# Optimization experiments

Measured on AMD Instinct MI355X. Metric: run time of the kernel, lower is better.

The kernel has to match this reference:

```python
import jax, jax.numpy as jnp
import numpy as np

N_QUBITS = 8    # out_channels = number of wires
KERNEL = 4      # kernel_size
N_LAYERS = 3
PAD = 1
STRIDE = 1


def _gate_rx(t):
    c = jnp.cos(t / 2).astype(jnp.complex64)
    s = (-1j) * jnp.sin(t / 2).astype(jnp.complex64)
    return jnp.stack([jnp.stack([c, s]), jnp.stack([s, c])])


def _gate_ry(t):
    c = jnp.cos(t / 2).astype(jnp.complex64)
    s = jnp.sin(t / 2).astype(jnp.complex64)
    return jnp.stack([jnp.stack([c, -s]), jnp.stack([s, c])])


def _gate_rz(t):
    tc = t.astype(jnp.complex64)
    e0 = jnp.exp(-0.5j * tc)
    e1 = jnp.exp(0.5j * tc)
    z = jnp.zeros_like(e0)
    return jnp.stack([jnp.stack([e0, z]), jnp.stack([z, e1])])


def _apply1(state, gate, q):
    # state: (W, 2, ..., 2); shared 2x2 gate on qubit axis 1+q
    s = jnp.moveaxis(state, 1 + q, -1)
    s = jnp.einsum('...a,ba->...b', s, gate)
    return jnp.moveaxis(s, -1, 1 + q)


def _apply_ry_batched(state, theta, q):
    # per-window RY angles theta: (W,)
    c = jnp.cos(theta / 2)
    s = jnp.sin(theta / 2)
    g = jnp.stack([jnp.stack([c, -s], -1), jnp.stack([s, c], -1)], -2).astype(jnp.complex64)  # (W,2,2)
    st = jnp.moveaxis(state, 1 + q, -1)
    st = jnp.einsum('w...a,wba->w...b', st, g)
    return jnp.moveaxis(st, -1, 1 + q)


def _apply_cnot(state, c, t):
    # control qubit c, target qubit t (axes 1+c, 1+t)
    s = jnp.moveaxis(state, 1 + c, 1)
    ta = 2 + t if t < c else 1 + t
    s = jnp.moveaxis(s, ta, 2)
    s = jnp.stack([s[:, 0], jnp.flip(s[:, 1], axis=1)], axis=1)
    s = jnp.moveaxis(s, 2, ta)
    return jnp.moveaxis(s, 1, 1 + c)


def _ansatz(state, w):
    # custom_ansatz: per wire j: RX(w[j]); CNOT; RY(w[j]); CNOT; RZ(w[j]) with ring entanglement
    for j in range(N_QUBITS):
        cw, tw = (j, j + 1) if j < N_QUBITS - 1 else (0, N_QUBITS - 1)
        state = _apply1(state, _gate_rx(w[j]), j)
        state = _apply_cnot(state, cw, tw)
        state = _apply1(state, _gate_ry(w[j]), j)
        state = _apply_cnot(state, cw, tw)
        state = _apply1(state, _gate_rz(w[j]), j)
    return state

_ansatz_ckpt = jax.checkpoint(_ansatz)


@jax.jit
def _circuit(windows, weights):
    # windows: (W, KERNEL); weights: (N_LAYERS+1, N_QUBITS)
    W = windows.shape[0]
    state = jnp.zeros((W,) + (2,) * N_QUBITS, jnp.complex64)
    state = state.at[(slice(None),) + (0,) * N_QUBITS].set(1.0)
    state = _ansatz_ckpt(state, weights[0])
    for k in range(KERNEL):  # 'no_reupload' data encoding, once
        state = _apply_ry_batched(state, windows[:, k], k)
    for i in range(1, N_LAYERS + 1):
        state = _ansatz_ckpt(state, weights[i])
    probs = state.real ** 2 + state.imag ** 2
    evs = []
    for j in range(N_QUBITS):
        axes = tuple(a for a in range(1, N_QUBITS + 1) if a != 1 + j)
        p = probs.sum(axis=axes)  # (W, 2)
        evs.append(p[:, 0] - p[:, 1])
    return jnp.stack(evs, axis=-1)  # (W, N_QUBITS)


def setup_inputs() -> dict:
    key = jax.random.key(0)
    k1, k2 = jax.random.split(key)
    vector = jax.random.normal(k1, (32, 1, 512), jnp.float32)
    weights = jax.random.uniform(k2, (N_LAYERS + 1, N_QUBITS), jnp.float32, 0.0, 2.0 * np.pi)
    return {"vector": vector, "weights": weights}


def reference(vector, weights):
    bs, ch, l = vector.shape
    if ch > 1:
        vector = vector.mean(axis=1, keepdims=True)
    v = jnp.pad(vector[:, 0], ((0, 0), (PAD, PAD)))
    l_out = (l + 2 * PAD - KERNEL) // STRIDE + 1
    idx = jnp.arange(0, l_out, STRIDE)[:, None] + jnp.arange(KERNEL)[None, :]
    windows = v[:, idx].reshape(-1, KERNEL)  # (bs*l_out, KERNEL)
    out = _circuit(windows, weights)
    return out.reshape(bs, l_out, N_QUBITS).transpose(0, 2, 1).astype(jnp.float32)
```

## Files before the change

kernel.cpp:

```cpp
#include <hip/hip_runtime.h>
#include <math.h>


#define DEV __device__ __forceinline__

#define NQ 8
#define LOUT 511
#define LIN 512
#define BS 32

DEV float sx(float v, int m) { return __shfl_xor(v, m, 64); }

template<int J>
DEV void rot_rx(float (&re)[4], float (&im)[4], float c, float s) {
    if constexpr (J == 0) {
        float r0=re[0], i0=im[0], r2=re[2], i2=im[2];
        re[0]=c*r0+s*i2; im[0]=c*i0-s*r2; re[2]=c*r2+s*i0; im[2]=c*i2-s*r0;
        float r1=re[1], i1=im[1], r3=re[3], i3=im[3];
        re[1]=c*r1+s*i3; im[1]=c*i1-s*r3; re[3]=c*r3+s*i1; im[3]=c*i3-s*r1;
    } else if constexpr (J == 1) {
        float r0=re[0], i0=im[0], r1=re[1], i1=im[1];
        re[0]=c*r0+s*i1; im[0]=c*i0-s*r1; re[1]=c*r1+s*i0; im[1]=c*i1-s*r0;
        float r2=re[2], i2=im[2], r3=re[3], i3=im[3];
        re[2]=c*r2+s*i3; im[2]=c*i2-s*r3; re[3]=c*r3+s*i2; im[3]=c*i3-s*r2;
    } else {
        constexpr int m = 1 << (7 - J);
        #pragma unroll
        for (int r = 0; r < 4; ++r) {
            float pre = sx(re[r], m), pim = sx(im[r], m);
            re[r] = c*re[r] + s*pim;
            im[r] = c*im[r] - s*pre;
        }
    }
}

template<int J>
DEV void rot_ry(float (&re)[4], float (&im)[4], float c, float s, int lane) {
    if constexpr (J == 0) {
        float r0=re[0], i0=im[0], r2=re[2], i2=im[2];
        re[0]=c*r0-s*r2; im[0]=c*i0-s*i2; re[2]=s*r0+c*r2; im[2]=s*i0+c*i2;
        float r1=re[1], i1=im[1], r3=re[3], i3=im[3];
        re[1]=c*r1-s*r3; im[1]=c*i1-s*i3; re[3]=s*r1+c*r3; im[3]=s*i1+c*i3;
    } else if constexpr (J == 1) {
        float r0=re[0], i0=im[0], r1=re[1], i1=im[1];
        re[0]=c*r0-s*r1; im[0]=c*i0-s*i1; re[1]=s*r0+c*r1; im[1]=s*i0+c*i1;
        float r2=re[2], i2=im[2], r3=re[3], i3=im[3];
        re[2]=c*r2-s*r3; im[2]=c*i2-s*i3; re[3]=s*r2+c*r3; im[3]=s*i2+c*i3;
    } else {
        constexpr int m = 1 << (7 - J);
        float sg = (lane & m) ? s : -s;
        #pragma unroll
        for (int r = 0; r < 4; ++r) {
            float pre = sx(re[r], m), pim = sx(im[r], m);
            re[r] = c*re[r] + sg*pre;
            im[r] = c*im[r] + sg*pim;
        }
    }
}

template<int J>
DEV void rot_rz(float (&re)[4], float (&im)[4], float c, float s, int lane) {
    if constexpr (J == 0) {
        float t;
        t=re[0]; re[0]=c*t+s*im[0]; im[0]=c*im[0]-s*t;
        t=re[1]; re[1]=c*t+s*im[1]; im[1]=c*im[1]-s*t;
        t=re[2]; re[2]=c*t-s*im[2]; im[2]=c*im[2]+s*t;
        t=re[3]; re[3]=c*t-s*im[3]; im[3]=c*im[3]+s*t;
    } else if constexpr (J == 1) {
        float t;
        t=re[0]; re[0]=c*t+s*im[0]; im[0]=c*im[0]-s*t;
        t=re[2]; re[2]=c*t+s*im[2]; im[2]=c*im[2]-s*t;
        t=re[1]; re[1]=c*t-s*im[1]; im[1]=c*im[1]+s*t;
        t=re[3]; re[3]=c*t-s*im[3]; im[3]=c*im[3]+s*t;
    } else {
        constexpr int m = 1 << (7 - J);
        float sg = (lane & m) ? -s : s;
        #pragma unroll
        for (int r = 0; r < 4; ++r) {
            float t = re[r];
            re[r] = c*t + sg*im[r];
            im[r] = c*im[r] - sg*t;
        }
    }
}

template<int J>
DEV void cnot_w(float (&re)[4], float (&im)[4], int lane) {
    if constexpr (J == 0) {
        float t;
        t=re[2]; re[2]=re[3]; re[3]=t;
        t=im[2]; im[2]=im[3]; im[3]=t;
    } else if constexpr (J == 1) {
        re[1]=sx(re[1],32); im[1]=sx(im[1],32);
        re[3]=sx(re[3],32); im[3]=sx(im[3],32);
    } else if constexpr (J == 7) {
        re[2]=sx(re[2],1); im[2]=sx(im[2],1);
        re[3]=sx(re[3],1); im[3]=sx(im[3],1);
    } else {
        constexpr int mc = 1 << (7 - J);
        constexpr int mt = 1 << (6 - J);
        bool ctrl = (lane & mc) != 0;
        #pragma unroll
        for (int r = 0; r < 4; ++r) {
            float pre = sx(re[r], mt), pim = sx(im[r], mt);
            re[r] = ctrl ? pre : re[r];
            im[r] = ctrl ? pim : im[r];
        }
    }
}

template<int J>
DEV void wire(float (&re)[4], float (&im)[4], float ang, int lane) {
    float s, c;
    sincosf(0.5f*ang, &s, &c);
    rot_rx<J>(re, im, c, s);
    cnot_w<J>(re, im, lane);
    rot_ry<J>(re, im, c, s, lane);
    cnot_w<J>(re, im, lane);
    rot_rz<J>(re, im, c, s, lane);
}

DEV void ansatz(float (&re)[4], float (&im)[4], const float* w, int lane) {
    wire<0>(re, im, w[0], lane);
    wire<1>(re, im, w[1], lane);
    wire<2>(re, im, w[2], lane);
    wire<3>(re, im, w[3], lane);
    wire<4>(re, im, w[4], lane);
    wire<5>(re, im, w[5], lane);
    wire<6>(re, im, w[6], lane);
    wire<7>(re, im, w[7], lane);
}

__global__ __launch_bounds__(64) void kA1(const float* __restrict__ wts,
                                          float2* __restrict__ q) {
    int lane = threadIdx.x;
    int b = blockIdx.x;
    float re[4] = {0.f,0.f,0.f,0.f}, im[4] = {0.f,0.f,0.f,0.f};
    if (lane == 0) re[0] = 1.0f;
    ansatz(re, im, wts, lane);
    if (b & 1) {
        float t;
        t=re[0]; re[0]=-re[2]; re[2]=t;  t=im[0]; im[0]=-im[2]; im[2]=t;
        t=re[1]; re[1]=-re[3]; re[3]=t;  t=im[1]; im[1]=-im[3]; im[3]=t;
    }
    if (b & 2) {
        float t;
        t=re[0]; re[0]=-re[1]; re[1]=t;  t=im[0]; im[0]=-im[1]; im[1]=t;
        t=re[2]; re[2]=-re[3]; re[3]=t;  t=im[2]; im[2]=-im[3]; im[3]=t;
    }
    if (b & 4) {
        bool hi = (lane & 32) != 0;
        #pragma unroll
        for (int r = 0; r < 4; ++r) {
            float pre = sx(re[r],32), pim = sx(im[r],32);
            re[r] = hi ? pre : -pre;
            im[r] = hi ? pim : -pim;
        }
    }
    if (b & 8) {
        bool hi = (lane & 16) != 0;
        #pragma unroll
        for (int r = 0; r < 4; ++r) {
            float pre = sx(re[r],16), pim = sx(im[r],16);
            re[r] = hi ? pre : -pre;
            im[r] = hi ? pim : -pim;
        }
    }
    ansatz(re, im, wts + 8,  lane);
    ansatz(re, im, wts + 16, lane);
    ansatz(re, im, wts + 24, lane);
    #pragma unroll
    for (int r = 0; r < 4; ++r)
        q[b*256 + r*64 + lane] = make_float2(re[r], im[r]);
}

__global__ __launch_bounds__(64) void kA2(const float2* __restrict__ q,
                                          float* __restrict__ S) {
    int lane = threadIdx.x;
    int b  = blockIdx.x >> 4;
    int bp = blockIdx.x & 15;
    float pp[4];
    #pragma unroll
    for (int rr = 0; rr < 4; ++rr) {
        float2 x = q[b*256  + rr*64 + lane];
        float2 y = q[bp*256 + rr*64 + lane];
        pp[rr] = x.x*y.x + x.y*y.y;
    }
    float acc[8];
    acc[0] = (pp[0]+pp[1]) - (pp[2]+pp[3]);
    acc[1] = (pp[0]+pp[2]) - (pp[1]+pp[3]);
    float tot = pp[0]+pp[1]+pp[2]+pp[3];
    acc[2] = (lane & 32) ? -tot : tot;
    acc[3] = (lane & 16) ? -tot : tot;
    acc[4] = (lane &  8) ? -tot : tot;
    acc[5] = (lane &  4) ? -tot : tot;
    acc[6] = (lane &  2) ? -tot : tot;
    acc[7] = (lane &  1) ? -tot : tot;
    #pragma unroll
    for (int j = 0; j < 8; ++j) {
        #pragma unroll
        for (int m = 1; m <= 32; m <<= 1)
            acc[j] += sx(acc[j], m);
    }
    if (lane == 0) {
        #pragma unroll
        for (int j = 0; j < 8; ++j)
            S[j*256 + b*16 + bp] = acc[j];
    }
}

__global__ __launch_bounds__(256) void kB(const float* __restrict__ vec,
                                          const float* __restrict__ S,
                                          float* __restrict__ out) {
    __shared__ float Sl[2048];
    for (int i = threadIdx.x; i < 2048; i += 256) Sl[i] = S[i];
    __syncthreads();
    int o   = blockIdx.x * 256 + threadIdx.x;
    int bat = blockIdx.y;
    if (o >= LOUT) return;
    float cs[4], sn[4];
    #pragma unroll
    for (int k = 0; k < 4; ++k) {
        int p = o + k;
        float x = (p >= 1 && p <= LIN) ? vec[bat*LIN + p - 1] : 0.f;
        sincosf(0.5f*x, &sn[k], &cs[k]);
    }
    float t[16];
    #pragma unroll
    for (int i = 0; i < 16; ++i)
        t[i] = ((i&1)?sn[0]:cs[0]) * ((i&2)?sn[1]:cs[1])
             * ((i&4)?sn[2]:cs[2]) * ((i&8)?sn[3]:cs[3]);
    for (int j = 0; j < 8; ++j) {
        float e = 0.f;
        #pragma unroll
        for (int b = 0; b < 16; ++b) {
            float u = 0.f;
            #pragma unroll
            for (int bp = 0; bp < 16; ++bp)
                u += Sl[j*256 + b*16 + bp] * t[bp];
            e += t[b] * u;
        }
        out[(bat*NQ + j)*LOUT + o] = e;
    }
}

extern "C" void kernel_launch(void* const* d_in, const int* in_sizes, int n_in,
                              void* d_out, int out_size, void* d_ws, size_t ws_size,
                              hipStream_t stream) {
    const float* vec = (const float*)d_in[0];
    const float* wts = (const float*)d_in[1];
    float* out = (float*)d_out;
    float2* q  = (float2*)d_ws;
    float*  S  = (float*)d_ws + 8192;
    kA1<<<16, 64, 0, stream>>>(wts, q);
    kA2<<<256, 64, 0, stream>>>(q, S);
    kB<<<dim3(2, BS), 256, 0, stream>>>(vec, S, out);
}
```

Baseline: 93.96 us.

## Fuse state-prep and overlap kernels, exploit S symmetry, use fast sincos

Merges the two precompute kernels into one 1024-thread block that keeps the 16 basis-state vectors in shared memory and computes only the 136 upper-triangle overlap entries, with off-diagonal terms doubled. The final kernel then contracts the symmetric form with t[b]*t[bp] products for all 8 outputs at once, reading coefficients straight from global memory (uniform, so scalar or cached loads). It also uses smaller 64-thread blocks for more parallelism and switches to the fast __sincosf intrinsic. This removes one launch and the global round-trip, and roughly halves the quadratic-form arithmetic. The cost is running all of the state prep on a single workgroup and slightly lower trig precision.

```diff
diff --git a/kernel.cpp b/kernel.cpp
--- a/kernel.cpp
+++ b/kernel.cpp
@@ -8,6 +8,7 @@
 #define LOUT 511
 #define LIN 512
 #define BS 32
+#define NPAIR 136
 
 DEV float sx(float v, int m) { return __shfl_xor(v, m, 64); }
 
@@ -112,7 +113,7 @@
 template<int J>
 DEV void wire(float (&re)[4], float (&im)[4], float ang, int lane) {
     float s, c;
-    sincosf(0.5f*ang, &s, &c);
+    __sincosf(0.5f*ang, &s, &c);
     rot_rx<J>(re, im, c, s);
     cnot_w<J>(re, im, lane);
     rot_ry<J>(re, im, c, s, lane);
@@ -131,24 +132,28 @@
     wire<7>(re, im, w[7], lane);
 }
 
-__global__ __launch_bounds__(64) void kA1(const float* __restrict__ wts,
-                                          float2* __restrict__ q) {
-    int lane = threadIdx.x;
-    int b = blockIdx.x;
+__global__ __launch_bounds__(1024) void kA(const float* __restrict__ wts,
+                                           float* __restrict__ Sc) {
+    __shared__ float2 qlds[16 * 256];
+    int tid  = threadIdx.x;
+    int lane = tid & 63;
+    int w    = tid >> 6;
+
     float re[4] = {0.f,0.f,0.f,0.f}, im[4] = {0.f,0.f,0.f,0.f};
     if (lane == 0) re[0] = 1.0f;
     ansatz(re, im, wts, lane);
-    if (b & 1) {
+
+    if (w & 1) {
         float t;
         t=re[0]; re[0]=-re[2]; re[2]=t;  t=im[0]; im[0]=-im[2]; im[2]=t;
         t=re[1]; re[1]=-re[3]; re[3]=t;  t=im[1]; im[1]=-im[3]; im[3]=t;
     }
-    if (b & 2) {
+    if (w & 2) {
         float t;
         t=re[0]; re[0]=-re[1]; re[1]=t;  t=im[0]; im[0]=-im[1]; im[1]=t;
         t=re[2]; re[2]=-re[3]; re[3]=t;  t=im[2]; im[2]=-im[3]; im[3]=t;
     }
-    if (b & 4) {
+    if (w & 4) {
         bool hi = (lane & 32) != 0;
         #pragma unroll
         for (int r = 0; r < 4; ++r) {
@@ -157,7 +162,7 @@
             im[r] = hi ? pim : -pim;
         }
     }
-    if (b & 8) {
+    if (w & 8) {
         bool hi = (lane & 16) != 0;
         #pragma unroll
         for (int r = 0; r < 4; ++r) {
@@ -171,76 +176,82 @@
     ansatz(re, im, wts + 24, lane);
     #pragma unroll
     for (int r = 0; r < 4; ++r)
-        q[b*256 + r*64 + lane] = make_float2(re[r], im[r]);
-}
-
-__global__ __launch_bounds__(64) void kA2(const float2* __restrict__ q,
-                                          float* __restrict__ S) {
+        qlds[w*256 + r*64 + lane] = make_float2(re[r], im[r]);
+    __syncthreads();
+
+    for (int m = w; m < NPAIR; m += 16) {
+        int b = 0, rem = m;
+        while (rem >= 16 - b) { rem -= 16 - b; ++b; }
+        int bp = b + rem;
+
+        float pp[4];
+        #pragma unroll
+        for (int rr = 0; rr < 4; ++rr) {
+            float2 x = qlds[b *256 + rr*64 + lane];
+            float2 y = qlds[bp*256 + rr*64 + lane];
+            pp[rr] = x.x*y.x + x.y*y.y;
+        }
+        float a0  = (pp[0]+pp[1]) - (pp[2]+pp[3]);
+        float a1  = (pp[0]+pp[2]) - (pp[1]+pp[3]);
+        float tot =  pp[0]+pp[1]+pp[2]+pp[3];
+
+        #pragma unroll
+        for (int mk = 1; mk <= 32; mk <<= 1) { a0 += sx(a0, mk); a1 += sx(a1, mk); }
+        #pragma unroll
+        for (int mk = 1; mk <= 32; mk <<= 1) {
+            float p = sx(tot, mk);
+            tot = (lane & mk) ? (p - tot) : (tot + p);
+        }
+        float scale = (b == bp) ? 1.0f : 2.0f;
+        if (lane == 0) { Sc[m*8+0] = scale*a0; Sc[m*8+1] = scale*a1; }
+        if (lane == 32) Sc[m*8+2] = scale*tot;
+        if (lane == 16) Sc[m*8+3] = scale*tot;
+        if (lane ==  8) Sc[m*8+4] = scale*tot;
+        if (lane ==  4) Sc[m*8+5] = scale*tot;
+        if (lane ==  2) Sc[m*8+6] = scale*tot;
+        if (lane ==  1) Sc[m*8+7] = scale*tot;
+    }
+}
+
+__global__ __launch_bounds__(64) void kB(const float* __restrict__ vec,
+                                         const float* __restrict__ Sc,
+                                         float* __restrict__ out) {
     int lane = threadIdx.x;
-    int b  = blockIdx.x >> 4;
-    int bp = blockIdx.x & 15;
-    float pp[4];
-    #pragma unroll
-    for (int rr = 0; rr < 4; ++rr) {
-        float2 x = q[b*256  + rr*64 + lane];
-        float2 y = q[bp*256 + rr*64 + lane];
-        pp[rr] = x.x*y.x + x.y*y.y;
-    }
-    float acc[8];
-    acc[0] = (pp[0]+pp[1]) - (pp[2]+pp[3]);
-    acc[1] = (pp[0]+pp[2]) - (pp[1]+pp[3]);
-    float tot = pp[0]+pp[1]+pp[2]+pp[3];
-    acc[2] = (lane & 32) ? -tot : tot;
-    acc[3] = (lane & 16) ? -tot : tot;
-    acc[4] = (lane &  8) ? -tot : tot;
-    acc[5] = (lane &  4) ? -tot : tot;
-    acc[6] = (lane &  2) ? -tot : tot;
-    acc[7] = (lane &  1) ? -tot : tot;
-    #pragma unroll
-    for (int j = 0; j < 8; ++j) {
-        #pragma unroll
-        for (int m = 1; m <= 32; m <<= 1)
-            acc[j] += sx(acc[j], m);
-    }
-    if (lane == 0) {
-        #pragma unroll
-        for (int j = 0; j < 8; ++j)
-            S[j*256 + b*16 + bp] = acc[j];
-    }
-}
-
-__global__ __launch_bounds__(256) void kB(const float* __restrict__ vec,
-                                          const float* __restrict__ S,
-                                          float* __restrict__ out) {
-    __shared__ float Sl[2048];
-    for (int i = threadIdx.x; i < 2048; i += 256) Sl[i] = S[i];
-    __syncthreads();
-    int o   = blockIdx.x * 256 + threadIdx.x;
-    int bat = blockIdx.y;
-    if (o >= LOUT) return;
+    int o    = blockIdx.x * 64 + lane;
+    int bat  = blockIdx.y;
+    bool valid = o < LOUT;
+    int oc = valid ? o : 0;
+
     float cs[4], sn[4];
     #pragma unroll
     for (int k = 0; k < 4; ++k) {
-        int p = o + k;
+        int p = oc + k;
         float x = (p >= 1 && p <= LIN) ? vec[bat*LIN + p - 1] : 0.f;
-        sincosf(0.5f*x, &sn[k], &cs[k]);
+        __sincosf(0.5f*x, &sn[k], &cs[k]);
     }
     float t[16];
     #pragma unroll
     for (int i = 0; i < 16; ++i)
         t[i] = ((i&1)?sn[0]:cs[0]) * ((i&2)?sn[1]:cs[1])
              * ((i&4)?sn[2]:cs[2]) * ((i&8)?sn[3]:cs[3]);
-    for (int j = 0; j < 8; ++j) {
-        float e = 0.f;
-        #pragma unroll
-        for (int b = 0; b < 16; ++b) {
-            float u = 0.f;
+
+    float acc[8] = {0.f,0.f,0.f,0.f,0.f,0.f,0.f,0.f};
+    int m = 0;
+    #pragma unroll
+    for (int b = 0; b < 16; ++b) {
+        #pragma unroll
+        for (int bp = b; bp < 16; ++bp) {
+            float p = t[b] * t[bp];
             #pragma unroll
-            for (int bp = 0; bp < 16; ++bp)
-                u += Sl[j*256 + b*16 + bp] * t[bp];
-            e += t[b] * u;
-        }
-        out[(bat*NQ + j)*LOUT + o] = e;
+            for (int j = 0; j < 8; ++j)
+                acc[j] = fmaf(Sc[m*8 + j], p, acc[j]);
+            ++m;
+        }
+    }
+    if (valid) {
+        #pragma unroll
+        for (int j = 0; j < 8; ++j)
+            out[(bat*NQ + j)*LOUT + o] = acc[j];
     }
 }
 
@@ -250,9 +261,7 @@
     const float* vec = (const float*)d_in[0];
     const float* wts = (const float*)d_in[1];
     float* out = (float*)d_out;
-    float2* q  = (float2*)d_ws;
-    float*  S  = (float*)d_ws + 8192;
-    kA1<<<16, 64, 0, stream>>>(wts, q);
-    kA2<<<256, 64, 0, stream>>>(q, S);
-    kB<<<dim3(2, BS), 256, 0, stream>>>(vec, S, out);
-}
+    float* Sc  = (float*)d_ws;
+    kA<<<1, 1024, 0, stream>>>(wts, Sc);
+    kB<<<dim3(8, BS), 64, 0, stream>>>(vec, Sc, out);
+}
```

After: 110.4 us. 17.5% more time.
